# Kernel tuning notes

Hardware: AMD Instinct MI355X
Metric: run time of the kernel (lower is better)

## Reference

```python
import jax, jax.numpy as jnp
import numpy as np

BS, L, SRC, E, H = 8, 1024, 1024, 768, 12
D = E // H  # head dim = 64


def setup_inputs() -> dict:
    key = jax.random.key(0)
    ks = jax.random.split(key, 12)
    p = lambda k, shp: (jax.random.normal(k, shp, jnp.float32) * 0.02)
    return {
        "query": jax.random.normal(ks[0], (BS, L, E), jnp.float32),
        "key": jax.random.normal(ks[1], (BS, SRC, E), jnp.float32),
        "value": jax.random.normal(ks[2], (BS, SRC, E), jnp.float32),
        "key_padding_mask": jax.random.uniform(ks[3], (BS, SRC), jnp.float32),
        "Wq": p(ks[4], (E, E)), "bq": jnp.zeros((E,), jnp.float32),
        "Wk": p(ks[5], (E, E)), "bk": jnp.zeros((E,), jnp.float32),
        "Wv": p(ks[6], (E, E)), "bv": jnp.zeros((E,), jnp.float32),
        "Wo": p(ks[7], (E, E)), "bo": jnp.zeros((E,), jnp.float32),
        "scaling_factors": jnp.array([-64, -64, -64, -32, -32, -32, -16, -16, -16, -8, -8, -8], jnp.float32),
    }


def reference(query, key, value, key_padding_mask, Wq, bq, Wk, bk, Wv, bv, Wo, bo, scaling_factors):
    bs = query.shape[0]
    # projections (torch Linear: x @ W.T + b)
    q = query @ Wq.T + bq          # [bs, L, E]
    k = key @ Wk.T + bk            # [bs, S, E]
    v = value @ Wv.T + bv          # [bs, S, E]
    # split heads
    q = q.reshape(bs, -1, H, D).transpose(0, 2, 1, 3)  # [bs, H, L, D]
    k = k.reshape(bs, -1, H, D).transpose(0, 2, 1, 3)  # [bs, H, S, D]
    v = v.reshape(bs, -1, H, D).transpose(0, 2, 1, 3)  # [bs, H, S, D]
    q = q / jnp.sqrt(jnp.float32(D))
    scores = jnp.einsum("bhld,bhsd->bhls", q, k)       # [bs, H, L, S]
    # soft key-padding bias: kpm[b,s] * scaling_factors[h]
    bias = key_padding_mask[:, None, None, :] * scaling_factors[None, :, None, None]
    scores = scores + bias
    attn = jax.nn.softmax(scores, axis=-1)             # dropout p=0 (eval)
    out = jnp.einsum("bhls,bhsd->bhld", attn, v)       # [bs, H, L, D]
    out = out.transpose(0, 2, 1, 3).reshape(bs, -1, E)  # [bs, L, E]
    return out @ Wo.T + bo
```

## Files before the change

kernel.cpp:

```cpp
#include <hip/hip_runtime.h>
#include <hip/hip_bf16.h>

typedef __attribute__((ext_vector_type(8))) short bf16x8;
typedef __attribute__((ext_vector_type(4))) float f32x4;

#define H_BS 8
#define H_L 1024
#define H_S 1024
#define H_E 768
#define H_NH 12
#define H_HD 64
#define EE (H_E * H_E)
#define AN (H_BS * H_L * H_E)

static __device__ __forceinline__ short cvtbf(float f) {
  __hip_bfloat16 h = __float2bfloat16(f);
  return *reinterpret_cast<short*>(&h);
}

static __device__ __forceinline__ void gload16(const void* g, void* l) {
  __builtin_amdgcn_global_load_lds(
      (const __attribute__((address_space(1))) void*)g,
      (__attribute__((address_space(3))) void*)l, 16, 0, 0);
}

__global__ __launch_bounds__(256)
void conv_bf16(const float* __restrict__ w0, const float* __restrict__ w1,
               const float* __restrict__ w2, const float* __restrict__ w3,
               const float* __restrict__ a0, const float* __restrict__ a1,
               const float* __restrict__ a2,
               short* __restrict__ ws_w, short* __restrict__ ws_a)
{
  const int y = blockIdx.y;
  const float* src;
  short* dst;
  int n;
  if (y < 4) {
    src = (y == 0) ? w0 : (y == 1) ? w1 : (y == 2) ? w2 : w3;
    dst = ws_w + (size_t)y * EE;
    n = EE;
  } else {
    src = (y == 4) ? a0 : (y == 5) ? a1 : a2;
    dst = ws_a + (size_t)(y - 4) * AN;
    n = AN;
  }
  const int i = (blockIdx.x * 256 + threadIdx.x) * 8;
  if (i >= n) return;
  const float4 f0 = *reinterpret_cast<const float4*>(src + i);
  const float4 f1 = *reinterpret_cast<const float4*>(src + i + 4);
  bf16x8 r;
  r[0] = cvtbf(f0.x); r[1] = cvtbf(f0.y); r[2] = cvtbf(f0.z); r[3] = cvtbf(f0.w);
  r[4] = cvtbf(f1.x); r[5] = cvtbf(f1.y); r[6] = cvtbf(f1.z); r[7] = cvtbf(f1.w);
  *reinterpret_cast<bf16x8*>(dst + i) = r;
}

__global__ __launch_bounds__(256)
void qkv_gemm(const short* __restrict__ Abf, const short* __restrict__ Wbf,
              const float* __restrict__ bq, const float* __restrict__ bk,
              const float* __restrict__ bv, short* __restrict__ oq,
              short* __restrict__ ok_, short* __restrict__ ov)
{
  __shared__ short a_s[128][32];
  __shared__ short w_s[128][32];

  const int mode = blockIdx.z;
  const short* A = Abf + (size_t)mode * AN;
  const short* W = Wbf + (size_t)mode * EE;
  const float* bias = (mode == 0) ? bq : (mode == 1) ? bk : bv;

  const int m0 = blockIdx.y * 128;
  const int n0 = blockIdx.x * 128;
  const int t = threadIdx.x;
  const int lane = t & 63;
  const int wv = t >> 6;
  const int wr = wv >> 1;
  const int wc = wv & 1;
  const int lr = lane & 15;
  const int lg = lane >> 4;

  f32x4 acc[4][4];
  const f32x4 zero = {0.f, 0.f, 0.f, 0.f};
  #pragma unroll
  for (int i = 0; i < 4; ++i)
    #pragma unroll
    for (int j = 0; j < 4; ++j) acc[i][j] = zero;

  const int g0 = wv * 2;
  const int srow = lane >> 2;
  const int scol = (lane & 3) * 8;
  const short* aptr0 = A + (size_t)(m0 + g0 * 16 + srow) * H_E + scol;
  const short* aptr1 = aptr0 + 16 * H_E;
  const short* wptr0 = W + (size_t)(n0 + g0 * 16 + srow) * H_E + scol;
  const short* wptr1 = wptr0 + 16 * H_E;
  short* adst0 = &a_s[0][0] + g0 * 512;
  short* adst1 = adst0 + 512;
  short* wdst0 = &w_s[0][0] + g0 * 512;
  short* wdst1 = wdst0 + 512;

  for (int kt = 0; kt < H_E / 32; ++kt) {
    const int ko = kt * 32;
    __syncthreads();
    gload16(aptr0 + ko, adst0);
    gload16(aptr1 + ko, adst1);
    gload16(wptr0 + ko, wdst0);
    gload16(wptr1 + ko, wdst1);
    __syncthreads();
    bf16x8 af[4], wf[4];
    #pragma unroll
    for (int i = 0; i < 4; ++i)
      af[i] = *reinterpret_cast<const bf16x8*>(&a_s[wr * 64 + i * 16 + lr][lg * 8]);
    #pragma unroll
    for (int j = 0; j < 4; ++j)
      wf[j] = *reinterpret_cast<const bf16x8*>(&w_s[wc * 64 + j * 16 + lr][lg * 8]);
    #pragma unroll
    for (int i = 0; i < 4; ++i)
      #pragma unroll
      for (int j = 0; j < 4; ++j)
        acc[i][j] = __builtin_amdgcn_mfma_f32_16x16x32_bf16(af[i], wf[j], acc[i][j], 0, 0, 0);
  }

  #pragma unroll
  for (int j = 0; j < 4; ++j) {
    const int gn = n0 + wc * 64 + j * 16 + lr;
    const float bvl = bias[gn];
    const int hh = gn >> 6, dd = gn & 63;
    #pragma unroll
    for (int i = 0; i < 4; ++i) {
      #pragma unroll
      for (int e = 0; e < 4; ++e) {
        const int gm = m0 + wr * 64 + i * 16 + lg * 4 + e;
        const float val = acc[i][j][e] + bvl;
        const int bb = gm >> 10, ll = gm & 1023;
        if (mode == 0)
          oq[((size_t)(bb * H_NH + hh) * H_L + ll) * H_HD + dd] = cvtbf(val * 0.125f);
        else if (mode == 1)
          ok_[((size_t)(bb * H_NH + hh) * H_S + ll) * H_HD + dd] = cvtbf(val);
        else
          ov[((size_t)(bb * H_NH + hh) * H_HD + dd) * H_S + ll] = cvtbf(val);
      }
    }
  }
}

__global__ __launch_bounds__(256)
void out_gemm(const short* __restrict__ A, const short* __restrict__ W,
              const float* __restrict__ bias, float* __restrict__ outp)
{
  __shared__ short a_s[128][32];
  __shared__ short w_s[128][32];

  const int m0 = blockIdx.y * 128;
  const int n0 = blockIdx.x * 128;
  const int t = threadIdx.x;
  const int lane = t & 63;
  const int wv = t >> 6;
  const int wr = wv >> 1;
  const int wc = wv & 1;
  const int lr = lane & 15;
  const int lg = lane >> 4;

  f32x4 acc[4][4];
  const f32x4 zero = {0.f, 0.f, 0.f, 0.f};
  #pragma unroll
  for (int i = 0; i < 4; ++i)
    #pragma unroll
    for (int j = 0; j < 4; ++j) acc[i][j] = zero;

  const int g0 = wv * 2;
  const int srow = lane >> 2;
  const int scol = (lane & 3) * 8;
  const short* aptr0 = A + (size_t)(m0 + g0 * 16 + srow) * H_E + scol;
  const short* aptr1 = aptr0 + 16 * H_E;
  const short* wptr0 = W + (size_t)(n0 + g0 * 16 + srow) * H_E + scol;
  const short* wptr1 = wptr0 + 16 * H_E;
  short* adst0 = &a_s[0][0] + g0 * 512;
  short* adst1 = adst0 + 512;
  short* wdst0 = &w_s[0][0] + g0 * 512;
  short* wdst1 = wdst0 + 512;

  for (int kt = 0; kt < H_E / 32; ++kt) {
    const int ko = kt * 32;
    __syncthreads();
    gload16(aptr0 + ko, adst0);
    gload16(aptr1 + ko, adst1);
    gload16(wptr0 + ko, wdst0);
    gload16(wptr1 + ko, wdst1);
    __syncthreads();
    bf16x8 af[4], wf[4];
    #pragma unroll
    for (int i = 0; i < 4; ++i)
      af[i] = *reinterpret_cast<const bf16x8*>(&a_s[wr * 64 + i * 16 + lr][lg * 8]);
    #pragma unroll
    for (int j = 0; j < 4; ++j)
      wf[j] = *reinterpret_cast<const bf16x8*>(&w_s[wc * 64 + j * 16 + lr][lg * 8]);
    #pragma unroll
    for (int i = 0; i < 4; ++i)
      #pragma unroll
      for (int j = 0; j < 4; ++j)
        acc[i][j] = __builtin_amdgcn_mfma_f32_16x16x32_bf16(af[i], wf[j], acc[i][j], 0, 0, 0);
  }

  #pragma unroll
  for (int j = 0; j < 4; ++j) {
    const int gn = n0 + wc * 64 + j * 16 + lr;
    const float bvl = bias[gn];
    #pragma unroll
    for (int i = 0; i < 4; ++i) {
      #pragma unroll
      for (int e = 0; e < 4; ++e) {
        const int gm = m0 + wr * 64 + i * 16 + lg * 4 + e;
        outp[(size_t)gm * H_E + gn] = acc[i][j][e] + bvl;
      }
    }
  }
}

__global__ __launch_bounds__(256)
void smha_attn(const short* __restrict__ q, const short* __restrict__ k,
               const short* __restrict__ vt, const float* __restrict__ kpm,
               const float* __restrict__ sf, short* __restrict__ outp)
{
  __shared__ short k_s[64][72];
  __shared__ short v_s[64][72];
  __shared__ short p_s[4][16][72];

  const int blk = blockIdx.x;
  const int qt = blk & 15;
  const int hh = (blk >> 4) % H_NH;
  const int bb = blk / (16 * H_NH);
  const int bh = bb * H_NH + hh;
  const int t = threadIdx.x;
  const int wv = t >> 6;
  const int lane = t & 63;
  const int lr = lane & 15;
  const int lg = lane >> 4;

  const int q0 = qt * 64 + wv * 16;

  bf16x8 qf[2];
  #pragma unroll
  for (int kk = 0; kk < 2; ++kk)
    qf[kk] = *reinterpret_cast<const bf16x8*>(
        &q[((size_t)bh * H_L + q0 + lr) * H_HD + kk * 32 + lg * 8]);

  const float sfh = sf[hh];

  f32x4 o_acc[4];
  const f32x4 zero = {0.f, 0.f, 0.f, 0.f};
  #pragma unroll
  for (int di = 0; di < 4; ++di) o_acc[di] = zero;
  float mrow[4], lrow[4];
  #pragma unroll
  for (int j = 0; j < 4; ++j) { mrow[j] = -1e30f; lrow[j] = 0.f; }

  const int srow = t >> 2;
  const int scol = (t & 3) * 16;

  const short* kp = &k[((size_t)bh * H_S + srow) * H_HD + scol];
  const short* vp = &vt[((size_t)bh * H_HD + srow) * H_S + scol];
  bf16x8 kr0 = *reinterpret_cast<const bf16x8*>(kp);
  bf16x8 kr1 = *reinterpret_cast<const bf16x8*>(kp + 8);
  bf16x8 vr0 = *reinterpret_cast<const bf16x8*>(vp);
  bf16x8 vr1 = *reinterpret_cast<const bf16x8*>(vp + 8);

  for (int kv = 0; kv < H_S / 64; ++kv) {
    const int s0 = kv * 64;
    __syncthreads();
    *reinterpret_cast<bf16x8*>(&k_s[srow][scol])     = kr0;
    *reinterpret_cast<bf16x8*>(&k_s[srow][scol + 8]) = kr1;
    *reinterpret_cast<bf16x8*>(&v_s[srow][scol])     = vr0;
    *reinterpret_cast<bf16x8*>(&v_s[srow][scol + 8]) = vr1;
    __syncthreads();
    if (kv + 1 < H_S / 64) {
      const short* kpn = kp + (size_t)(kv + 1) * 64 * H_HD;
      const short* vpn = vp + (size_t)(kv + 1) * 64;
      kr0 = *reinterpret_cast<const bf16x8*>(kpn);
      kr1 = *reinterpret_cast<const bf16x8*>(kpn + 8);
      vr0 = *reinterpret_cast<const bf16x8*>(vpn);
      vr1 = *reinterpret_cast<const bf16x8*>(vpn + 8);
    }

    float bias_c[4];
    #pragma unroll
    for (int ni = 0; ni < 4; ++ni)
      bias_c[ni] = kpm[bb * H_S + s0 + ni * 16 + lr] * sfh;

    f32x4 sc[4];
    #pragma unroll
    for (int ni = 0; ni < 4; ++ni) sc[ni] = zero;
    #pragma unroll
    for (int kk = 0; kk < 2; ++kk) {
      #pragma unroll
      for (int ni = 0; ni < 4; ++ni) {
        const bf16x8 bfr = *reinterpret_cast<const bf16x8*>(&k_s[ni * 16 + lr][kk * 32 + lg * 8]);
        sc[ni] = __builtin_amdgcn_mfma_f32_16x16x32_bf16(qf[kk], bfr, sc[ni], 0, 0, 0);
      }
    }

    #pragma unroll
    for (int j = 0; j < 4; ++j) {
      float mx = -1e30f;
      #pragma unroll
      for (int ni = 0; ni < 4; ++ni) {
        sc[ni][j] += bias_c[ni];
        mx = fmaxf(mx, sc[ni][j]);
      }
      mx = fmaxf(mx, __shfl_xor(mx, 1));
      mx = fmaxf(mx, __shfl_xor(mx, 2));
      mx = fmaxf(mx, __shfl_xor(mx, 4));
      mx = fmaxf(mx, __shfl_xor(mx, 8));
      if (!__all(mx <= mrow[j] + 8.0f)) {
        const float mnew = fmaxf(mrow[j], mx);
        const float scal = __expf(mrow[j] - mnew);
        lrow[j] *= scal;
        #pragma unroll
        for (int di = 0; di < 4; ++di) o_acc[di][j] *= scal;
        mrow[j] = mnew;
      }
      float rsum = 0.f;
      #pragma unroll
      for (int ni = 0; ni < 4; ++ni) {
        const float p = __expf(sc[ni][j] - mrow[j]);
        sc[ni][j] = p;
        rsum += p;
      }
      rsum += __shfl_xor(rsum, 1);
      rsum += __shfl_xor(rsum, 2);
      rsum += __shfl_xor(rsum, 4);
      rsum += __shfl_xor(rsum, 8);
      lrow[j] += rsum;
    }

    #pragma unroll
    for (int ni = 0; ni < 4; ++ni)
      #pragma unroll
      for (int j = 0; j < 4; ++j)
        p_s[wv][lg * 4 + j][ni * 16 + lr] = cvtbf(sc[ni][j]);

    #pragma unroll
    for (int kk = 0; kk < 2; ++kk) {
      const bf16x8 pf = *reinterpret_cast<const bf16x8*>(&p_s[wv][lr][kk * 32 + lg * 8]);
      #pragma unroll
      for (int di = 0; di < 4; ++di) {
        const bf16x8 vfr = *reinterpret_cast<const bf16x8*>(&v_s[di * 16 + lr][kk * 32 + lg * 8]);
        o_acc[di] = __builtin_amdgcn_mfma_f32_16x16x32_bf16(pf, vfr, o_acc[di], 0, 0, 0);
      }
    }
  }

  #pragma unroll
  for (int j = 0; j < 4; ++j) {
    const float rl = 1.0f / lrow[j];
    const int gq = q0 + lg * 4 + j;
    #pragma unroll
    for (int di = 0; di < 4; ++di)
      outp[((size_t)bb * H_L + gq) * H_E + hh * H_HD + di * 16 + lr] =
          cvtbf(o_acc[di][j] * rl);
  }
}

extern "C" void kernel_launch(void* const* d_in, const int* in_sizes, int n_in,
                              void* d_out, int out_size, void* d_ws, size_t ws_size,
                              hipStream_t stream)
{
  short* ws_w  = (short*)d_ws;
  short* ws_a  = ws_w + (size_t)4 * EE;
  short* ws_q  = ws_a + (size_t)3 * AN;
  short* ws_k  = ws_q + AN;
  short* ws_vt = ws_k + AN;
  short* ws_at = ws_a;

  conv_bf16<<<dim3(AN / 2048, 7), 256, 0, stream>>>(
      (const float*)d_in[4], (const float*)d_in[6], (const float*)d_in[8],
      (const float*)d_in[10], (const float*)d_in[0], (const float*)d_in[1],
      (const float*)d_in[2], ws_w, ws_a);

  qkv_gemm<<<dim3(H_E / 128, (H_BS * H_L) / 128, 3), 256, 0, stream>>>(
      ws_a, ws_w, (const float*)d_in[5], (const float*)d_in[7],
      (const float*)d_in[9], ws_q, ws_k, ws_vt);

  smha_attn<<<H_BS * H_NH * (H_L / 64), 256, 0, stream>>>(
      ws_q, ws_k, ws_vt, (const float*)d_in[3], (const float*)d_in[12], ws_at);

  out_gemm<<<dim3(H_E / 128, (H_BS * H_L) / 128), 256, 0, stream>>>(
      ws_at, ws_w + (size_t)3 * EE, (const float*)d_in[11], (float*)d_out);
}
```

Baseline: 319.3 us.

## Transpose score MFMA, fold log2e into Q scaling, use exp2 softmax

Swaps the operands of the QK^T MFMA so each lane holds one query row's scores across keys. This makes the row max and sum reductions mostly in-register, with only two cross-lane shuffles instead of four per row. Log2(e) is folded into the Q projection scale and the head bias so the softmax can use native exp2. The bias is loaded as a vector straight into the accumulator init, and P is written to LDS as packed bf16x4 stores. The rescale threshold is adjusted to base 2, and the output correction factors and the final normaliser need extra shuffles to redistribute per-row state.

```diff
diff --git a/kernel.cpp b/kernel.cpp
--- a/kernel.cpp
+++ b/kernel.cpp
@@ -2,6 +2,7 @@
 #include <hip/hip_bf16.h>
 
 typedef __attribute__((ext_vector_type(8))) short bf16x8;
+typedef __attribute__((ext_vector_type(4))) short bf16x4;
 typedef __attribute__((ext_vector_type(4))) float f32x4;
 
 #define H_BS 8
@@ -12,10 +13,19 @@
 #define H_HD 64
 #define EE (H_E * H_E)
 #define AN (H_BS * H_L * H_E)
+#define LOG2E 1.44269504f
 
 static __device__ __forceinline__ short cvtbf(float f) {
   __hip_bfloat16 h = __float2bfloat16(f);
   return *reinterpret_cast<short*>(&h);
+}
+
+static __device__ __forceinline__ float fexp2(float x) {
+#if __has_builtin(__builtin_amdgcn_exp2f)
+  return __builtin_amdgcn_exp2f(x);
+#else
+  return __expf(x * 0.69314718056f);
+#endif
 }
 
 static __device__ __forceinline__ void gload16(const void* g, void* l) {
@@ -132,7 +142,7 @@
         const float val = acc[i][j][e] + bvl;
         const int bb = gm >> 10, ll = gm & 1023;
         if (mode == 0)
-          oq[((size_t)(bb * H_NH + hh) * H_L + ll) * H_HD + dd] = cvtbf(val * 0.125f);
+          oq[((size_t)(bb * H_NH + hh) * H_L + ll) * H_HD + dd] = cvtbf(val * (0.125f * LOG2E));
         else if (mode == 1)
           ok_[((size_t)(bb * H_NH + hh) * H_S + ll) * H_HD + dd] = cvtbf(val);
         else
@@ -243,15 +253,14 @@
     qf[kk] = *reinterpret_cast<const bf16x8*>(
         &q[((size_t)bh * H_L + q0 + lr) * H_HD + kk * 32 + lg * 8]);
 
-  const float sfh = sf[hh];
+  const float sfh = sf[hh] * LOG2E;
+  const float* kpmb = kpm + bb * H_S;
 
   f32x4 o_acc[4];
   const f32x4 zero = {0.f, 0.f, 0.f, 0.f};
   #pragma unroll
   for (int di = 0; di < 4; ++di) o_acc[di] = zero;
-  float mrow[4], lrow[4];
-  #pragma unroll
-  for (int j = 0; j < 4; ++j) { mrow[j] = -1e30f; lrow[j] = 0.f; }
+  float mrow = -1e30f, lrow = 0.f;
 
   const int srow = t >> 2;
   const int scol = (t & 3) * 16;
@@ -280,62 +289,63 @@
       vr1 = *reinterpret_cast<const bf16x8*>(vpn + 8);
     }
 
-    float bias_c[4];
+    f32x4 sc[4];
+    #pragma unroll
+    for (int ni = 0; ni < 4; ++ni) {
+      const f32x4 kp4 = *reinterpret_cast<const f32x4*>(&kpmb[s0 + ni * 16 + lg * 4]);
+      #pragma unroll
+      for (int e = 0; e < 4; ++e) sc[ni][e] = kp4[e] * sfh;
+    }
+    #pragma unroll
+    for (int kk = 0; kk < 2; ++kk) {
+      #pragma unroll
+      for (int ni = 0; ni < 4; ++ni) {
+        const bf16x8 kf = *reinterpret_cast<const bf16x8*>(&k_s[ni * 16 + lr][kk * 32 + lg * 8]);
+        sc[ni] = __builtin_amdgcn_mfma_f32_16x16x32_bf16(kf, qf[kk], sc[ni], 0, 0, 0);
+      }
+    }
+
+    float pm[4];
     #pragma unroll
     for (int ni = 0; ni < 4; ++ni)
-      bias_c[ni] = kpm[bb * H_S + s0 + ni * 16 + lr] * sfh;
-
-    f32x4 sc[4];
-    #pragma unroll
-    for (int ni = 0; ni < 4; ++ni) sc[ni] = zero;
-    #pragma unroll
-    for (int kk = 0; kk < 2; ++kk) {
-      #pragma unroll
-      for (int ni = 0; ni < 4; ++ni) {
-        const bf16x8 bfr = *reinterpret_cast<const bf16x8*>(&k_s[ni * 16 + lr][kk * 32 + lg * 8]);
-        sc[ni] = __builtin_amdgcn_mfma_f32_16x16x32_bf16(qf[kk], bfr, sc[ni], 0, 0, 0);
-      }
-    }
-
-    #pragma unroll
-    for (int j = 0; j < 4; ++j) {
-      float mx = -1e30f;
-      #pragma unroll
-      for (int ni = 0; ni < 4; ++ni) {
-        sc[ni][j] += bias_c[ni];
-        mx = fmaxf(mx, sc[ni][j]);
-      }
-      mx = fmaxf(mx, __shfl_xor(mx, 1));
-      mx = fmaxf(mx, __shfl_xor(mx, 2));
-      mx = fmaxf(mx, __shfl_xor(mx, 4));
-      mx = fmaxf(mx, __shfl_xor(mx, 8));
-      if (!__all(mx <= mrow[j] + 8.0f)) {
-        const float mnew = fmaxf(mrow[j], mx);
-        const float scal = __expf(mrow[j] - mnew);
-        lrow[j] *= scal;
+      pm[ni] = fmaxf(fmaxf(sc[ni][0], sc[ni][1]), fmaxf(sc[ni][2], sc[ni][3]));
+    float mx = fmaxf(fmaxf(pm[0], pm[1]), fmaxf(pm[2], pm[3]));
+    mx = fmaxf(mx, __shfl_xor(mx, 16));
+    mx = fmaxf(mx, __shfl_xor(mx, 32));
+
+    if (!__all(mx <= mrow + 11.5f)) {
+      const float mnew = fmaxf(mrow, mx);
+      const float scal = fexp2(mrow - mnew);
+      lrow *= scal;
+      float sj[4];
+      #pragma unroll
+      for (int j = 0; j < 4; ++j) sj[j] = __shfl(scal, lg * 4 + j);
+      #pragma unroll
+      for (int di = 0; di < 4; ++di)
         #pragma unroll
-        for (int di = 0; di < 4; ++di) o_acc[di][j] *= scal;
-        mrow[j] = mnew;
-      }
-      float rsum = 0.f;
-      #pragma unroll
-      for (int ni = 0; ni < 4; ++ni) {
-        const float p = __expf(sc[ni][j] - mrow[j]);
-        sc[ni][j] = p;
-        rsum += p;
-      }
-      rsum += __shfl_xor(rsum, 1);
-      rsum += __shfl_xor(rsum, 2);
-      rsum += __shfl_xor(rsum, 4);
-      rsum += __shfl_xor(rsum, 8);
-      lrow[j] += rsum;
-    }
-
-    #pragma unroll
-    for (int ni = 0; ni < 4; ++ni)
-      #pragma unroll
-      for (int j = 0; j < 4; ++j)
-        p_s[wv][lg * 4 + j][ni * 16 + lr] = cvtbf(sc[ni][j]);
+        for (int j = 0; j < 4; ++j) o_acc[di][j] *= sj[j];
+      mrow = mnew;
+    }
+
+    float ps[4];
+    #pragma unroll
+    for (int ni = 0; ni < 4; ++ni) {
+      #pragma unroll
+      for (int e = 0; e < 4; ++e) sc[ni][e] = fexp2(sc[ni][e] - mrow);
+      ps[ni] = (sc[ni][0] + sc[ni][1]) + (sc[ni][2] + sc[ni][3]);
+    }
+    float rs = (ps[0] + ps[1]) + (ps[2] + ps[3]);
+    rs += __shfl_xor(rs, 16);
+    rs += __shfl_xor(rs, 32);
+    lrow += rs;
+
+    #pragma unroll
+    for (int ni = 0; ni < 4; ++ni) {
+      bf16x4 pk4;
+      pk4[0] = cvtbf(sc[ni][0]); pk4[1] = cvtbf(sc[ni][1]);
+      pk4[2] = cvtbf(sc[ni][2]); pk4[3] = cvtbf(sc[ni][3]);
+      *reinterpret_cast<bf16x4*>(&p_s[wv][lr][ni * 16 + lg * 4]) = pk4;
+    }
 
     #pragma unroll
     for (int kk = 0; kk < 2; ++kk) {
@@ -350,7 +360,7 @@
 
   #pragma unroll
   for (int j = 0; j < 4; ++j) {
-    const float rl = 1.0f / lrow[j];
+    const float rl = 1.0f / __shfl(lrow, lg * 4 + j);
     const int gq = q0 + lg * 4 + j;
     #pragma unroll
     for (int di = 0; di < 4; ++di)
```

Result: faster. 290.0 us (-9.2%).
